# Optimization experiments

Hardware: AMD Instinct MI355X
Metric: run time of the kernel (lower is better)

Reference implementation:

```python
import jax, jax.numpy as jnp
import numpy as np

D_MODEL = 1024
NUM_HEADS = 16
DEPTH = D_MODEL // NUM_HEADS
B, S = 2, 2048


def setup_inputs() -> dict:
    key = jax.random.key(0)
    ks = jax.random.split(key, 8)
    scale = 1.0 / np.sqrt(D_MODEL)
    return {
        "v": jax.random.normal(ks[0], (B, S, D_MODEL), jnp.float32),
        "k": jax.random.normal(ks[1], (B, S, D_MODEL), jnp.float32),
        "q": jax.random.normal(ks[2], (B, S, D_MODEL), jnp.float32),
        "mask": jnp.zeros((B, 1, 1, S), jnp.float32),
        "wq": jax.random.normal(ks[3], (D_MODEL, D_MODEL), jnp.float32) * scale,
        "wk": jax.random.normal(ks[4], (D_MODEL, D_MODEL), jnp.float32) * scale,
        "wv": jax.random.normal(ks[5], (D_MODEL, D_MODEL), jnp.float32) * scale,
        "wo": jax.random.normal(ks[6], (D_MODEL, D_MODEL), jnp.float32) * scale,
        "bq": jnp.zeros((D_MODEL,), jnp.float32),
        "bk": jnp.zeros((D_MODEL,), jnp.float32),
        "bv": jnp.zeros((D_MODEL,), jnp.float32),
        "bo": jnp.zeros((D_MODEL,), jnp.float32),
    }


def _split_heads(x):
    # [B, S, d_model] -> [B, H, S, depth]
    b, s, _ = x.shape
    return x.reshape(b, s, NUM_HEADS, DEPTH).transpose(0, 2, 1, 3)


def reference(v, k, q, mask, wq, wk, wv, wo, bq, bk, bv, bo):
    qh = _split_heads(q @ wq + bq)
    kh = _split_heads(k @ wk + bk)
    vh = _split_heads(v @ wv + bv)
    # scores: [B, H, Sq, Sk]
    scores = jnp.einsum("bhqd,bhkd->bhqk", qh, kh) / jnp.sqrt(
        jnp.asarray(DEPTH, jnp.float32))
    scores = scores + mask * -1e9
    attn = jax.nn.softmax(scores, axis=-1)
    out = jnp.einsum("bhqk,bhkd->bhqd", attn, vh)  # [B, H, Sq, depth]
    out = out.transpose(0, 2, 1, 3).reshape(q.shape[0], -1, D_MODEL)
    out = out @ wo + bo
    return out, attn
```

## Files before the change

kernel.cpp:

```cpp
#include <hip/hip_runtime.h>

#define S_LEN 2048
#define DM 1024
#define NH 16
#define DH 64

typedef __attribute__((ext_vector_type(8))) short short8;
typedef __attribute__((ext_vector_type(4))) float f32x4;
typedef unsigned short u16;
typedef unsigned int u32;

__device__ __forceinline__ u16 f2b(float f){
  union { float f; u32 u; } v; v.f = f;
  return (u16)((v.u + 0x7fffu + ((v.u >> 16) & 1u)) >> 16);
}

__device__ __forceinline__ f32x4 mfma16(short8 a, short8 b, f32x4 c){
  return __builtin_amdgcn_mfma_f32_16x16x32_bf16(a, b, c, 0, 0, 0);
}

template<int R>
__device__ __forceinline__ void stage_tile(const u16* src, int ld, u16* lds){
  const int t = threadIdx.x;
  #pragma unroll
  for (int it = 0; it < R/32; ++it){
    int idx = it*256 + t;
    int row = idx >> 3;
    int ch  = (idx & 7) ^ (row & 7);
    const u16* g = src + row*ld + ch*8;
    u16* l = lds + (it*256 + (t & ~63))*8;
    __builtin_amdgcn_global_load_lds((const __attribute__((address_space(1))) void*)g,
                                     (__attribute__((address_space(3))) void*)l, 16, 0, 0);
  }
}

__device__ __forceinline__ short8 frag_ld(const u16* tile, int row, int ch){
  int off = (row*128 + ch*16) ^ ((row & 7) << 4);
  return *(const short8*)((const char*)tile + off);
}

__global__ __launch_bounds__(256) void k_cast(
    const float* __restrict__ q, const float* __restrict__ k, const float* __restrict__ v,
    u16* __restrict__ qb, u16* __restrict__ kb, u16* __restrict__ vb)
{
  int z = blockIdx.z;
  const float* src = (z==0)?q:(z==1)?k:v;
  u16* dst = (z==0)?qb:(z==1)?kb:vb;
  long i = ((long)blockIdx.x*256 + threadIdx.x)*8;
  f32x4 a = *(const f32x4*)(src + i);
  f32x4 b = *(const f32x4*)(src + i + 4);
  short8 o;
  #pragma unroll
  for (int j = 0; j < 4; ++j){ o[j] = (short)f2b(a[j]); o[4+j] = (short)f2b(b[j]); }
  *(short8*)(dst + i) = o;
}

__global__ __launch_bounds__(256) void k_transpose(
    const float* __restrict__ wq, const float* __restrict__ wk,
    const float* __restrict__ wv, const float* __restrict__ wo,
    u16* __restrict__ oq, u16* __restrict__ ok, u16* __restrict__ ov, u16* __restrict__ oo)
{
  int z = blockIdx.z;
  const float* W = (z==0)?wq:(z==1)?wk:(z==2)?wv:wo;
  u16* O = (z==0)?oq:(z==1)?ok:(z==2)?ov:oo;
  int k0 = blockIdx.x*64, n0 = blockIdx.y*64;
  __shared__ float tl[64][65];
  int t = threadIdx.x;
  #pragma unroll
  for (int i = 0; i < 16; ++i){
    int idx = i*256 + t;
    int row = idx >> 6, col = idx & 63;
    tl[row][col] = W[(long)(k0+row)*DM + n0 + col];
  }
  __syncthreads();
  #pragma unroll
  for (int i = 0; i < 16; ++i){
    int idx = i*256 + t;
    int n = idx >> 6, kk = idx & 63;
    O[(long)(n0+n)*DM + k0 + kk] = f2b(tl[kk][n]);
  }
}

__device__ __forceinline__ void gemm_body(const u16* __restrict__ X, const u16* __restrict__ WT,
    const float* __restrict__ bias, u16* __restrict__ dst16, float* __restrict__ dst32,
    int layout, int m0, int n0, u16* At, u16* Bt)
{
  const int t = threadIdx.x, lane = t & 63, w = t >> 6;
  const int wr = (w >> 1) * 64, wc = (w & 1) * 64;
  const int li = lane & 15, lg = lane >> 4;
  const f32x4 zero = {0.f, 0.f, 0.f, 0.f};
  f32x4 acc[4][4];
  #pragma unroll
  for (int m = 0; m < 4; ++m)
    #pragma unroll
    for (int n = 0; n < 4; ++n) acc[m][n] = zero;

  for (int kt = 0; kt < DM/64; ++kt){
    stage_tile<128>(X  + (long)m0*DM + kt*64, DM, At);
    stage_tile<128>(WT + (long)n0*DM + kt*64, DM, Bt);
    __syncthreads();
    #pragma unroll
    for (int ks = 0; ks < 2; ++ks){
      int ch = ks*4 + lg;
      short8 a[4], b[4];
      #pragma unroll
      for (int m = 0; m < 4; ++m) a[m] = frag_ld(At, wr + m*16 + li, ch);
      #pragma unroll
      for (int n = 0; n < 4; ++n) b[n] = frag_ld(Bt, wc + n*16 + li, ch);
      #pragma unroll
      for (int m = 0; m < 4; ++m)
        #pragma unroll
        for (int n = 0; n < 4; ++n) acc[m][n] = mfma16(a[m], b[n], acc[m][n]);
    }
    __syncthreads();
  }

  if (layout == 1){
    f32x4 bm[4];
    #pragma unroll
    for (int m = 0; m < 4; ++m) bm[m] = *(const f32x4*)(bias + m0 + wr + m*16 + lg*4);
    #pragma unroll
    for (int m = 0; m < 4; ++m)
      #pragma unroll
      for (int n = 0; n < 4; ++n)
        #pragma unroll
        for (int r = 0; r < 4; ++r){
          int gm = m0 + wr + m*16 + lg*4 + r;
          int gc = n0 + wc + n*16 + li;
          int hh = gm >> 6, dd = gm & 63, bb = gc >> 11, ss = gc & (S_LEN-1);
          dst16[(((long)(bb*NH + hh))*DH + dd)*S_LEN + ss] = f2b(acc[m][n][r] + bm[m][r]);
        }
  } else {
    float bv4[4];
    #pragma unroll
    for (int n = 0; n < 4; ++n) bv4[n] = bias[n0 + wc + n*16 + li];
    #pragma unroll
    for (int m = 0; m < 4; ++m)
      #pragma unroll
      for (int n = 0; n < 4; ++n)
        #pragma unroll
        for (int r = 0; r < 4; ++r){
          int gm = m0 + wr + m*16 + lg*4 + r;
          int gc = n0 + wc + n*16 + li;
          float val = acc[m][n][r] + bv4[n];
          if (layout == 0){
            int bb = gm >> 11, ss = gm & (S_LEN-1), hh = gc >> 6, dd = gc & 63;
            dst16[(((long)(bb*NH + hh))*S_LEN + ss)*DH + dd] = f2b(val);
          } else {
            dst32[(long)gm*DM + gc] = val;
          }
        }
  }
}

__global__ __launch_bounds__(256) void k_gemm_qkv(
    const u16* __restrict__ qb, const u16* __restrict__ kb, const u16* __restrict__ vb,
    const u16* __restrict__ wtq, const u16* __restrict__ wtk, const u16* __restrict__ wtv,
    const float* __restrict__ bq, const float* __restrict__ bk, const float* __restrict__ bv,
    u16* __restrict__ Qw, u16* __restrict__ Kw, u16* __restrict__ VTw)
{
  __shared__ u16 At[128*64], Bt[128*64];
  int z = blockIdx.z;
  if (z == 2){
    gemm_body(wtv, vb, bv, VTw, nullptr, 1, blockIdx.y*128, blockIdx.x*128, At, Bt);
  } else {
    const u16* X  = (z==0)?qb:kb;
    const u16* WT = (z==0)?wtq:wtk;
    const float* B = (z==0)?bq:bk;
    u16* dst = (z==0)?Qw:Kw;
    gemm_body(X, WT, B, dst, nullptr, 0, blockIdx.x*128, blockIdx.y*128, At, Bt);
  }
}

__global__ __launch_bounds__(256) void k_gemm_out(
    const u16* __restrict__ ctx, const u16* __restrict__ wto,
    const float* __restrict__ bo, float* __restrict__ out)
{
  __shared__ u16 At[128*64], Bt[128*64];
  gemm_body(ctx, wto, bo, nullptr, out, 2, blockIdx.x*128, blockIdx.y*128, At, Bt);
}

__global__ __launch_bounds__(256) void k_attn1(const u16* __restrict__ Q, const u16* __restrict__ K,
    const float* __restrict__ mask, float* __restrict__ mrow, float* __restrict__ lrow)
{
  __shared__ u16 Kt[2][64*64];
  const int t = threadIdx.x, lane = t & 63, w = t >> 6;
  const int li = lane & 15, lg = lane >> 4;
  const int q0 = blockIdx.x*64, bh = blockIdx.y, b = bh >> 4;
  const u16* Qb = Q + ((long)bh*S_LEN + q0 + w*16 + li)*DH;
  short8 qa0 = *(const short8*)(Qb + lg*8);
  short8 qa1 = *(const short8*)(Qb + 32 + lg*8);
  float m = -3.0e38f, l = 0.f;

  stage_tile<64>(K + (long)bh*S_LEN*DH, DH, Kt[0]);
  __syncthreads();
  for (int tt = 0; tt < S_LEN/64; ++tt){
    const u16* cur = Kt[tt & 1];
    if (tt + 1 < S_LEN/64)
      stage_tile<64>(K + ((long)bh*S_LEN + (tt+1)*64)*DH, DH, Kt[(tt+1) & 1]);
    float sv[4][4];
    #pragma unroll
    for (int c = 0; c < 4; ++c){
      f32x4 acc = {0.f,0.f,0.f,0.f};
      acc = mfma16(frag_ld(cur, c*16 + li, lg),     qa0, acc);
      acc = mfma16(frag_ld(cur, c*16 + li, 4 + lg), qa1, acc);
      f32x4 mk = *(const f32x4*)(mask + b*S_LEN + tt*64 + c*16 + lg*4);
      #pragma unroll
      for (int r = 0; r < 4; ++r) sv[c][r] = acc[r]*0.125f - 1e9f*mk[r];
    }
    float tm = -3.0e38f;
    #pragma unroll
    for (int c = 0; c < 4; ++c)
      tm = fmaxf(tm, fmaxf(fmaxf(sv[c][0], sv[c][1]), fmaxf(sv[c][2], sv[c][3])));
    tm = fmaxf(tm, __shfl_xor(tm, 16));
    tm = fmaxf(tm, __shfl_xor(tm, 32));
    float mn = fmaxf(m, tm);
    float ps = 0.f;
    #pragma unroll
    for (int c = 0; c < 4; ++c)
      #pragma unroll
      for (int r = 0; r < 4; ++r) ps += __expf(sv[c][r] - mn);
    ps += __shfl_xor(ps, 16);
    ps += __shfl_xor(ps, 32);
    l = l*__expf(m - mn) + ps;
    m = mn;
    __syncthreads();
  }
  if (lane < 16){
    mrow[bh*S_LEN + q0 + w*16 + li] = m;
    lrow[bh*S_LEN + q0 + w*16 + li] = l;
  }
}

__global__ __launch_bounds__(256) void k_attn2(const u16* __restrict__ Q, const u16* __restrict__ K,
    const u16* __restrict__ VT, const float* __restrict__ mask,
    const float* __restrict__ mrow, const float* __restrict__ lrow,
    float* __restrict__ attn, u16* __restrict__ ctx)
{
  __shared__ u16 Kt[2][64*64], Vt[2][64*64], Pt[64*64];
  const int t = threadIdx.x, lane = t & 63, w = t >> 6;
  const int li = lane & 15, lg = lane >> 4;
  const int q0 = blockIdx.x*64, bh = blockIdx.y, b = bh >> 4;
  const u16* Qb = Q + ((long)bh*S_LEN + q0 + w*16 + li)*DH;
  short8 qa0 = *(const short8*)(Qb + lg*8);
  short8 qa1 = *(const short8*)(Qb + 32 + lg*8);
  const float m  = mrow[bh*S_LEN + q0 + w*16 + li];
  const float rl = 1.f / lrow[bh*S_LEN + q0 + w*16 + li];
  float rle[4];
  #pragma unroll
  for (int r = 0; r < 4; ++r)
    rle[r] = 1.f / lrow[bh*S_LEN + q0 + w*16 + lg*4 + r];
  const f32x4 zero = {0.f,0.f,0.f,0.f};
  f32x4 cacc[4];
  #pragma unroll
  for (int c2 = 0; c2 < 4; ++c2) cacc[c2] = zero;
  float* arow = attn + ((long)bh*S_LEN + q0 + w*16 + li)*S_LEN;
  const int prow = w*16 + li;
  const int pswz = (prow & 7) << 4;

  stage_tile<64>(K  + (long)bh*S_LEN*DH, DH, Kt[0]);
  stage_tile<64>(VT + (long)bh*DH*S_LEN, S_LEN, Vt[0]);
  __syncthreads();
  for (int tt = 0; tt < S_LEN/64; ++tt){
    const int cur = tt & 1;
    if (tt + 1 < S_LEN/64){
      stage_tile<64>(K  + ((long)bh*S_LEN + (tt+1)*64)*DH, DH, Kt[cur^1]);
      stage_tile<64>(VT + (long)bh*DH*S_LEN + (tt+1)*64, S_LEN, Vt[cur^1]);
    }
    #pragma unroll
    for (int c = 0; c < 4; ++c){
      f32x4 acc = {0.f,0.f,0.f,0.f};
      acc = mfma16(frag_ld(Kt[cur], c*16 + li, lg),     qa0, acc);
      acc = mfma16(frag_ld(Kt[cur], c*16 + li, 4 + lg), qa1, acc);
      f32x4 mk = *(const f32x4*)(mask + b*S_LEN + tt*64 + c*16 + lg*4);
      f32x4 pv, av;
      #pragma unroll
      for (int r = 0; r < 4; ++r){
        pv[r] = __expf(acc[r]*0.125f - 1e9f*mk[r] - m);
        av[r] = pv[r] * rl;
      }
      *(f32x4*)(arow + tt*64 + c*16 + lg*4) = av;
      uint2 pu;
      pu.x = (u32)f2b(pv[0]) | ((u32)f2b(pv[1]) << 16);
      pu.y = (u32)f2b(pv[2]) | ((u32)f2b(pv[3]) << 16);
      int off = (prow*128 + (c*16 + lg*4)*2) ^ pswz;
      *(uint2*)((char*)Pt + off) = pu;
    }
    #pragma unroll
    for (int ks = 0; ks < 2; ++ks){
      short8 pa = frag_ld(Pt, prow, ks*4 + lg);
      #pragma unroll
      for (int c2 = 0; c2 < 4; ++c2)
        cacc[c2] = mfma16(pa, frag_ld(Vt[cur], c2*16 + li, ks*4 + lg), cacc[c2]);
    }
    __syncthreads();
  }
  int bb = bh >> 4, hh = bh & 15;
  #pragma unroll
  for (int c2 = 0; c2 < 4; ++c2)
    #pragma unroll
    for (int r = 0; r < 4; ++r){
      float val = cacc[c2][r] * rle[r];
      ctx[((long)bb*S_LEN + q0 + w*16 + lg*4 + r)*DM + hh*DH + c2*16 + li] = f2b(val);
    }
}

extern "C" void kernel_launch(void* const* d_in, const int* in_sizes, int n_in,
                              void* d_out, int out_size, void* d_ws, size_t ws_size,
                              hipStream_t stream)
{
  const float* v_in = (const float*)d_in[0];
  const float* k_in = (const float*)d_in[1];
  const float* q_in = (const float*)d_in[2];
  const float* mask = (const float*)d_in[3];
  const float* wq = (const float*)d_in[4];
  const float* wk = (const float*)d_in[5];
  const float* wv = (const float*)d_in[6];
  const float* wo = (const float*)d_in[7];
  const float* bq = (const float*)d_in[8];
  const float* bk = (const float*)d_in[9];
  const float* bv = (const float*)d_in[10];
  const float* bo = (const float*)d_in[11];

  float* out  = (float*)d_out;
  float* attn = out + (long)2*S_LEN*DM;

  char* ws = (char*)d_ws;
  const long MW = 1024*1024;
  u16*  wtq = (u16*)(ws);
  u16*  wtk = (u16*)(ws + 2*MW);
  u16*  wtv = (u16*)(ws + 4*MW);
  u16*  wto = (u16*)(ws + 6*MW);
  u16*  qb  = (u16*)(ws + 8*MW);
  u16*  kb  = (u16*)(ws + 17*MW);
  u16*  vb  = (u16*)(ws + 26*MW);
  u16*  Qw  = (u16*)(ws + 35*MW);
  u16*  Kw  = (u16*)(ws + 44*MW);
  u16*  VTw = (u16*)(ws + 53*MW);
  u16*  ctx = (u16*)(ws + 8*MW);
  float* mrow = (float*)(ws + 17*MW);
  float* lrow = (float*)(ws + 18*MW);

  k_cast<<<dim3(2048,1,3), 256, 0, stream>>>(q_in, k_in, v_in, qb, kb, vb);
  k_transpose<<<dim3(16,16,4), 256, 0, stream>>>(wq,wk,wv,wo, wtq,wtk,wtv,wto);
  k_gemm_qkv<<<dim3(32,8,3), 256, 0, stream>>>(qb,kb,vb, wtq,wtk,wtv, bq,bk,bv, Qw,Kw,VTw);
  k_attn1<<<dim3(32,32), 256, 0, stream>>>(Qw, Kw, mask, mrow, lrow);
  k_attn2<<<dim3(32,32), 256, 0, stream>>>(Qw, Kw, VTw, mask, mrow, lrow, attn, ctx);
  k_gemm_out<<<dim3(32,8), 256, 0, stream>>>(ctx, wto, bo, out);
}
```

Measured before the change: 350.5 us.

## Fuse attention passes into one kernel and remap blocks for XCD locality

Merges the two attention kernels, the max/sum pass and the probability/context pass, into a single kernel. The row max and sum stay in registers instead of going through global mrow/lrow buffers, which saves one launch and a global round trip. It also linearizes the grids of the QKV GEMM, the output GEMM and attention, so that blocks landing on the same XCD share M tiles or heads and get better L2 reuse. Shared memory per block grows to the larger footprint for the whole kernel, and both passes over K still run.

New measurement: 355.1 us. No clear change (+1.3%).

```diff
diff --git a/kernel.cpp b/kernel.cpp
--- a/kernel.cpp
+++ b/kernel.cpp
@@ -160,15 +160,18 @@
     u16* __restrict__ Qw, u16* __restrict__ Kw, u16* __restrict__ VTw)
 {
   __shared__ u16 At[128*64], Bt[128*64];
-  int z = blockIdx.z;
+  int bid = blockIdx.x;
+  int xcd = bid & 7, j = bid >> 3;
+  int z = j >> 5, tt = j & 31;
+  int mi = xcd*4 + (tt >> 3), n = tt & 7;
   if (z == 2){
-    gemm_body(wtv, vb, bv, VTw, nullptr, 1, blockIdx.y*128, blockIdx.x*128, At, Bt);
+    gemm_body(wtv, vb, bv, VTw, nullptr, 1, n*128, mi*128, At, Bt);
   } else {
     const u16* X  = (z==0)?qb:kb;
     const u16* WT = (z==0)?wtq:wtk;
     const float* B = (z==0)?bq:bk;
     u16* dst = (z==0)?Qw:Kw;
-    gemm_body(X, WT, B, dst, nullptr, 0, blockIdx.x*128, blockIdx.y*128, At, Bt);
+    gemm_body(X, WT, B, dst, nullptr, 0, mi*128, n*128, At, Bt);
   }
 }
 
@@ -177,21 +180,30 @@
     const float* __restrict__ bo, float* __restrict__ out)
 {
   __shared__ u16 At[128*64], Bt[128*64];
-  gemm_body(ctx, wto, bo, nullptr, out, 2, blockIdx.x*128, blockIdx.y*128, At, Bt);
-}
-
-__global__ __launch_bounds__(256) void k_attn1(const u16* __restrict__ Q, const u16* __restrict__ K,
-    const float* __restrict__ mask, float* __restrict__ mrow, float* __restrict__ lrow)
-{
-  __shared__ u16 Kt[2][64*64];
+  int bid = blockIdx.x;
+  int xcd = bid & 7, tt = bid >> 3;
+  int mi = xcd*4 + (tt >> 3), n = tt & 7;
+  gemm_body(ctx, wto, bo, nullptr, out, 2, mi*128, n*128, At, Bt);
+}
+
+__global__ __launch_bounds__(256) void k_attn(const u16* __restrict__ Q, const u16* __restrict__ K,
+    const u16* __restrict__ VT, const float* __restrict__ mask,
+    float* __restrict__ attn, u16* __restrict__ ctx)
+{
+  __shared__ u16 Kt[2][64*64], Vt[2][64*64], Pt[64*64];
   const int t = threadIdx.x, lane = t & 63, w = t >> 6;
   const int li = lane & 15, lg = lane >> 4;
-  const int q0 = blockIdx.x*64, bh = blockIdx.y, b = bh >> 4;
+  int bid = blockIdx.x;
+  int xcd = bid & 7, j = bid >> 3;
+  int bh = xcd + 8*(j & 3);
+  int q0 = (j >> 2) * 64;
+  int b = bh >> 4;
   const u16* Qb = Q + ((long)bh*S_LEN + q0 + w*16 + li)*DH;
   short8 qa0 = *(const short8*)(Qb + lg*8);
   short8 qa1 = *(const short8*)(Qb + 32 + lg*8);
+  const float* mrow_g = mask + b*S_LEN;
+
   float m = -3.0e38f, l = 0.f;
-
   stage_tile<64>(K + (long)bh*S_LEN*DH, DH, Kt[0]);
   __syncthreads();
   for (int tt = 0; tt < S_LEN/64; ++tt){
@@ -204,7 +216,7 @@
       f32x4 acc = {0.f,0.f,0.f,0.f};
       acc = mfma16(frag_ld(cur, c*16 + li, lg),     qa0, acc);
       acc = mfma16(frag_ld(cur, c*16 + li, 4 + lg), qa1, acc);
-      f32x4 mk = *(const f32x4*)(mask + b*S_LEN + tt*64 + c*16 + lg*4);
+      f32x4 mk = *(const f32x4*)(mrow_g + tt*64 + c*16 + lg*4);
       #pragma unroll
       for (int r = 0; r < 4; ++r) sv[c][r] = acc[r]*0.125f - 1e9f*mk[r];
     }
@@ -226,30 +238,13 @@
     m = mn;
     __syncthreads();
   }
-  if (lane < 16){
-    mrow[bh*S_LEN + q0 + w*16 + li] = m;
-    lrow[bh*S_LEN + q0 + w*16 + li] = l;
-  }
-}
-
-__global__ __launch_bounds__(256) void k_attn2(const u16* __restrict__ Q, const u16* __restrict__ K,
-    const u16* __restrict__ VT, const float* __restrict__ mask,
-    const float* __restrict__ mrow, const float* __restrict__ lrow,
-    float* __restrict__ attn, u16* __restrict__ ctx)
-{
-  __shared__ u16 Kt[2][64*64], Vt[2][64*64], Pt[64*64];
-  const int t = threadIdx.x, lane = t & 63, w = t >> 6;
-  const int li = lane & 15, lg = lane >> 4;
-  const int q0 = blockIdx.x*64, bh = blockIdx.y, b = bh >> 4;
-  const u16* Qb = Q + ((long)bh*S_LEN + q0 + w*16 + li)*DH;
-  short8 qa0 = *(const short8*)(Qb + lg*8);
-  short8 qa1 = *(const short8*)(Qb + 32 + lg*8);
-  const float m  = mrow[bh*S_LEN + q0 + w*16 + li];
-  const float rl = 1.f / lrow[bh*S_LEN + q0 + w*16 + li];
+
+  const float rl = 1.f / l;
   float rle[4];
   #pragma unroll
   for (int r = 0; r < 4; ++r)
-    rle[r] = 1.f / lrow[bh*S_LEN + q0 + w*16 + lg*4 + r];
+    rle[r] = 1.f / __shfl(l, (lane & 48) + lg*4 + r);
+
   const f32x4 zero = {0.f,0.f,0.f,0.f};
   f32x4 cacc[4];
   #pragma unroll
@@ -272,7 +267,7 @@
       f32x4 acc = {0.f,0.f,0.f,0.f};
       acc = mfma16(frag_ld(Kt[cur], c*16 + li, lg),     qa0, acc);
       acc = mfma16(frag_ld(Kt[cur], c*16 + li, 4 + lg), qa1, acc);
-      f32x4 mk = *(const f32x4*)(mask + b*S_LEN + tt*64 + c*16 + lg*4);
+      f32x4 mk = *(const f32x4*)(mrow_g + tt*64 + c*16 + lg*4);
       f32x4 pv, av;
       #pragma unroll
       for (int r = 0; r < 4; ++r){
@@ -338,13 +333,10 @@
   u16*  Kw  = (u16*)(ws + 44*MW);
   u16*  VTw = (u16*)(ws + 53*MW);
   u16*  ctx = (u16*)(ws + 8*MW);
-  float* mrow = (float*)(ws + 17*MW);
-  float* lrow = (float*)(ws + 18*MW);
 
   k_cast<<<dim3(2048,1,3), 256, 0, stream>>>(q_in, k_in, v_in, qb, kb, vb);
   k_transpose<<<dim3(16,16,4), 256, 0, stream>>>(wq,wk,wv,wo, wtq,wtk,wtv,wto);
-  k_gemm_qkv<<<dim3(32,8,3), 256, 0, stream>>>(qb,kb,vb, wtq,wtk,wtv, bq,bk,bv, Qw,Kw,VTw);
-  k_attn1<<<dim3(32,32), 256, 0, stream>>>(Qw, Kw, mask, mrow, lrow);
-  k_attn2<<<dim3(32,32), 256, 0, stream>>>(Qw, Kw, VTw, mask, mrow, lrow, attn, ctx);
-  k_gemm_out<<<dim3(32,8), 256, 0, stream>>>(ctx, wto, bo, out);
-}
+  k_gemm_qkv<<<768, 256, 0, stream>>>(qb,kb,vb, wtq,wtk,wtv, bq,bk,bv, Qw,Kw,VTw);
+  k_attn<<<1024, 256, 0, stream>>>(Qw, Kw, VTw, mask, attn, ctx);
+  k_gemm_out<<<256, 256, 0, stream>>>(ctx, wto, bo, out);
+}
```
